# Performance work log

Hardware: AMD Instinct MI355X
Metric: run time of the kernel (lower is better)

Reference implementation:

```python
import jax, jax.numpy as jnp
import numpy as np

HIDDEN = 1024
HEADS = 16
HEAD_DIM = HIDDEN // HEADS
B, S = 2, 2048


def setup_inputs() -> dict:
    key = jax.random.key(0)
    ks = jax.random.split(key, 11)
    std = 1.0 / np.sqrt(HIDDEN)
    return {
        "query": jax.random.normal(ks[0], (B, S, HIDDEN), dtype=jnp.float32),
        "key": jax.random.normal(ks[1], (B, S, HIDDEN), dtype=jnp.float32),
        "value": jax.random.normal(ks[2], (B, S, HIDDEN), dtype=jnp.float32),
        "Wq": jax.random.uniform(ks[3], (HIDDEN, HIDDEN), jnp.float32, -std, std),
        "bq": jax.random.uniform(ks[4], (HIDDEN,), jnp.float32, -std, std),
        "Wk": jax.random.uniform(ks[5], (HIDDEN, HIDDEN), jnp.float32, -std, std),
        "bk": jax.random.uniform(ks[6], (HIDDEN,), jnp.float32, -std, std),
        "Wv": jax.random.uniform(ks[7], (HIDDEN, HIDDEN), jnp.float32, -std, std),
        "bv": jax.random.uniform(ks[8], (HIDDEN,), jnp.float32, -std, std),
        "Wo": jax.random.uniform(ks[9], (HIDDEN, HIDDEN), jnp.float32, -std, std),
        "bo": jax.random.uniform(ks[10], (HIDDEN,), jnp.float32, -std, std),
    }


def reference(query, key, value, Wq, bq, Wk, bk, Wv, bv, Wo, bo):
    b = query.shape[0]
    scale = jnp.sqrt(jnp.float32(HEAD_DIM))
    # linear projections (torch Linear: x @ W.T + b), split into heads -> [b, h, s, d]
    def proj(x, W, bias):
        y = x @ W.T + bias
        return y.reshape(b, -1, HEADS, HEAD_DIM).transpose(0, 2, 1, 3)
    Q = proj(query, Wq, bq)
    K = proj(key, Wk, bk)
    V = proj(value, Wv, bv)
    scores = jnp.einsum("bhqd,bhkd->bhqk", Q, K) / scale
    attn = jax.nn.softmax(scores, axis=-1)
    ctx = jnp.einsum("bhqk,bhkd->bhqd", attn, V)
    ctx = ctx.transpose(0, 2, 1, 3).reshape(b, -1, HIDDEN)
    return ctx @ Wo.T + bo
```

## Files before the change

### kernel.cpp

```cpp
#include <hip/hip_runtime.h>

typedef __attribute__((ext_vector_type(8))) short short8;
typedef __attribute__((ext_vector_type(4))) float float4_t;
typedef __attribute__((ext_vector_type(4))) unsigned int uint4_t;
typedef __attribute__((ext_vector_type(2))) unsigned int uint2_t;
typedef unsigned short u16;

#define HIDDEN 1024
#define HDIM   64
#define SS     2048
#define TOK    4096
#define QSCALE 0.1803368801111137f

__device__ __forceinline__ unsigned int fbits(float f) {
  unsigned int x; __builtin_memcpy(&x, &f, 4); return x;
}
__device__ __forceinline__ u16 f2bf(float f) {
  return (u16)((fbits(f) + 0x8000u) >> 16);
}
__device__ __forceinline__ unsigned int pk2bf(float a, float b) {
  return __builtin_amdgcn_perm(fbits(b) + 0x8000u, fbits(a) + 0x8000u, 0x07060302);
}
__device__ __forceinline__ unsigned int pk2bf_t(float a, float b) {
  return __builtin_amdgcn_perm(fbits(b), fbits(a), 0x07060302);
}

__device__ __forceinline__ void gl_lds16(const u16* g, u16* l) {
  __builtin_amdgcn_global_load_lds(
      (const __attribute__((address_space(1))) unsigned int*)g,
      (__attribute__((address_space(3))) unsigned int*)l, 16, 0, 0);
}

__global__ __launch_bounds__(256) void convert_w(
    const float* __restrict__ w0, const float* __restrict__ w1,
    const float* __restrict__ w2, const float* __restrict__ w3,
    u16* __restrict__ out) {
  int g = (blockIdx.x * 256 + threadIdx.x) * 8;
  int which = g >> 20;
  int off = g & 0xFFFFF;
  const float* src = which == 0 ? w0 : which == 1 ? w1 : which == 2 ? w2 : w3;
  float4_t a = *(const float4_t*)(src + off);
  float4_t b = *(const float4_t*)(src + off + 4);
  uint4_t o;
  o.x = pk2bf(a[0], a[1]); o.y = pk2bf(a[2], a[3]);
  o.z = pk2bf(b[0], b[1]); o.w = pk2bf(b[2], b[3]);
  *(uint4_t*)(out + g) = o;
}

__global__ __launch_bounds__(256) void convert_x(
    const float* __restrict__ x0, const float* __restrict__ x1,
    const float* __restrict__ x2, u16* __restrict__ out) {
  int y = blockIdx.y;
  const float* src = y == 0 ? x0 : y == 1 ? x1 : x2;
  u16* dst = out + ((size_t)y << 22);
  int g = (blockIdx.x * 256 + threadIdx.x) * 8;
  float4_t a = *(const float4_t*)(src + g);
  float4_t b = *(const float4_t*)(src + g + 4);
  uint4_t o;
  o.x = pk2bf(a[0], a[1]); o.y = pk2bf(a[2], a[3]);
  o.z = pk2bf(b[0], b[1]); o.w = pk2bf(b[2], b[3]);
  *(uint4_t*)(dst + g) = o;
}

template<int MTILES, bool AXF32, bool OUTF32>
__device__ __forceinline__ void gemm_bt_body(
    const void* __restrict__ X, const u16* __restrict__ Wb,
    const float* __restrict__ bias, void* __restrict__ Y, int mode, float oscale,
    u16* sA, u16* sB, int row0, int col0) {
  const int tid  = threadIdx.x;
  const int wv   = tid >> 6, lane = tid & 63, quad = lane >> 4, ln = lane & 15;
  const int wm   = (wv >> 1) * (MTILES * 16), wn = (wv & 1) * 64;
  constexpr int AITERS = MTILES / 2;

  float4_t acc[MTILES][4];
#pragma unroll
  for (int i = 0; i < MTILES; i++)
#pragma unroll
    for (int j = 0; j < 4; j++) acc[i][j] = (float4_t)0.0f;

  for (int kt = 0; kt < 32; ++kt) {
    const int k0 = kt * 32;
    short8 ax[AITERS];
    if (AXF32) {
#pragma unroll
      for (int i = 0; i < AITERS; i++) {
        int idx = i * 256 + tid, r = idx >> 2, c = idx & 3;
        const float* p = (const float*)X + (size_t)(row0 + r) * HIDDEN + k0 + c * 8;
        float4_t a = *(const float4_t*)p;
        float4_t b = *(const float4_t*)(p + 4);
        union { unsigned int u[4]; short8 s; } x;
        x.u[0] = pk2bf(a[0], a[1]); x.u[1] = pk2bf(a[2], a[3]);
        x.u[2] = pk2bf(b[0], b[1]); x.u[3] = pk2bf(b[2], b[3]);
        ax[i] = x.s;
      }
    }
    __syncthreads();
#pragma unroll
    for (int i = 0; i < 2; i++) {
      int idx = i * 256 + tid, r = idx >> 2, c = idx & 3;
      int gc = c ^ ((r >> 1) & 3);
      gl_lds16(Wb + (size_t)(col0 + r) * HIDDEN + k0 + gc * 8, sB + idx * 8);
    }
    if (AXF32) {
#pragma unroll
      for (int i = 0; i < AITERS; i++) {
        int idx = i * 256 + tid, r = idx >> 2, c = idx & 3;
        int pos = c ^ ((r >> 1) & 3);
        *(short8*)(sA + r * 32 + pos * 8) = ax[i];
      }
    } else {
#pragma unroll
      for (int i = 0; i < AITERS; i++) {
        int idx = i * 256 + tid, r = idx >> 2, c = idx & 3;
        int gc = c ^ ((r >> 1) & 3);
        gl_lds16((const u16*)X + (size_t)(row0 + r) * HIDDEN + k0 + gc * 8, sA + idx * 8);
      }
    }
    __syncthreads();

    short8 af[MTILES], bfr[4];
#pragma unroll
    for (int mt = 0; mt < MTILES; mt++) {
      int r = wm + mt * 16 + ln;
      int pos = quad ^ ((r >> 1) & 3);
      af[mt] = *(const short8*)(sA + r * 32 + pos * 8);
    }
#pragma unroll
    for (int nt = 0; nt < 4; nt++) {
      int r = wn + nt * 16 + ln;
      int pos = quad ^ ((r >> 1) & 3);
      bfr[nt] = *(const short8*)(sB + r * 32 + pos * 8);
    }
#pragma unroll
    for (int mt = 0; mt < MTILES; mt++)
#pragma unroll
      for (int nt = 0; nt < 4; nt++)
        acc[mt][nt] = __builtin_amdgcn_mfma_f32_16x16x32_bf16(af[mt], bfr[nt], acc[mt][nt], 0, 0, 0);
  }

  float bcol[4];
#pragma unroll
  for (int nt = 0; nt < 4; nt++) bcol[nt] = bias[col0 + wn + nt * 16 + ln];
#pragma unroll
  for (int mt = 0; mt < MTILES; mt++)
#pragma unroll
    for (int nt = 0; nt < 4; nt++) {
      int n = col0 + wn + nt * 16 + ln;
#pragma unroll
      for (int r = 0; r < 4; r++) {
        int m = row0 + wm + mt * 16 + quad * 4 + r;
        float v = (acc[mt][nt][r] + bcol[nt]) * oscale;
        if (mode == 0) {
          if (OUTF32) ((float*)Y)[(size_t)m * HIDDEN + n] = v;
          else        ((u16*)Y)[(size_t)m * HIDDEN + n] = f2bf(v);
        } else {
          ((u16*)Y)[((size_t)(m >> 11) * HIDDEN + n) * SS + (m & 2047)] = f2bf(v);
        }
      }
    }
}

__global__ __launch_bounds__(256) void qkv_gemm_bf16(
    const u16* __restrict__ Xall, const u16* __restrict__ Wall,
    const float* __restrict__ bq, const float* __restrict__ bk, const float* __restrict__ bv,
    u16* __restrict__ Qp, u16* __restrict__ Kp, u16* __restrict__ Vt) {
  __shared__ u16 sA[128 * 32];
  __shared__ u16 sB[128 * 32];
  int z = blockIdx.z;
  const u16* X = Xall + ((size_t)z << 22);
  const u16* W = Wall + ((size_t)z << 20);
  const float* Bp = z == 0 ? bq : z == 1 ? bk : bv;
  u16* Y = z == 0 ? Qp : z == 1 ? Kp : Vt;
  int mode = (z == 2) ? 1 : 0;
  float sc = (z == 0) ? QSCALE : 1.0f;
  gemm_bt_body<4, false, false>(X, W, Bp, Y, mode, sc, sA, sB, blockIdx.y * 128, blockIdx.x * 128);
}

__global__ __launch_bounds__(256) void qkv_gemm_f32(
    const float* __restrict__ xq, const float* __restrict__ xk, const float* __restrict__ xv,
    const u16* __restrict__ Wall,
    const float* __restrict__ bq, const float* __restrict__ bk, const float* __restrict__ bv,
    u16* __restrict__ Qp, u16* __restrict__ Kp, u16* __restrict__ Vt) {
  __shared__ u16 sA[128 * 32];
  __shared__ u16 sB[128 * 32];
  int z = blockIdx.z;
  const float* X = z == 0 ? xq : z == 1 ? xk : xv;
  const u16* W = Wall + ((size_t)z << 20);
  const float* Bp = z == 0 ? bq : z == 1 ? bk : bv;
  u16* Y = z == 0 ? Qp : z == 1 ? Kp : Vt;
  int mode = (z == 2) ? 1 : 0;
  float sc = (z == 0) ? QSCALE : 1.0f;
  gemm_bt_body<4, true, false>(X, W, Bp, Y, mode, sc, sA, sB, blockIdx.y * 128, blockIdx.x * 128);
}

__global__ __launch_bounds__(256) void out_gemm(
    const u16* __restrict__ X, const u16* __restrict__ Wob,
    const float* __restrict__ bias, float* __restrict__ Y) {
  __shared__ u16 sA[64 * 32];
  __shared__ u16 sB[128 * 32];
  gemm_bt_body<2, false, true>(X, Wob, bias, Y, 0, 1.0f, sA, sB, blockIdx.y * 64, blockIdx.x * 128);
}

__global__ __launch_bounds__(256) void attn(
    const u16* __restrict__ Qp, const u16* __restrict__ Kp,
    const u16* __restrict__ Vt, u16* __restrict__ Ctx) {
  __shared__ u16 sK[128 * 64];
  __shared__ u16 sV[80 * 128];
  __shared__ u16 sP[4 * 32 * 64];
  const int tid  = threadIdx.x;
  const int wv   = tid >> 6, lane = tid & 63, quad = lane >> 4, ln = lane & 15;
  const int qt = blockIdx.x, h = blockIdx.y, b = blockIdx.z;
  const int row0 = qt * 128 + wv * 32;

  {
    int rr = 64 + (tid >> 4), cc = (tid & 15) * 8;
    short8 vv;
#pragma unroll
    for (int j = 0; j < 8; j++) vv[j] = (rr == 64) ? (short)0x3F80 : (short)0;
    *(short8*)(sV + rr * 128 + cc) = vv;
  }

  short8 qf[2][2];
#pragma unroll
  for (int j = 0; j < 2; j++)
#pragma unroll
    for (int kk = 0; kk < 2; kk++)
      qf[j][kk] = *(const short8*)(Qp + (size_t)(b * SS + row0 + j * 16 + ln) * HIDDEN
                                   + h * HDIM + kk * 32 + quad * 8);

  float4_t oacc[2][5];
#pragma unroll
  for (int j = 0; j < 2; j++)
#pragma unroll
    for (int t = 0; t < 5; t++) oacc[j][t] = (float4_t)0.f;

  u16* myP = sP + wv * 32 * 64;

  for (int kt = 0; kt < 16; ++kt) {
    __syncthreads();
#pragma unroll
    for (int p = 0; p < 4; p++) {
      int off = p * 256 + tid;
      { int r = off >> 3, c = off & 7;  int gc = c ^ (r & 7);
        gl_lds16(Kp + (size_t)(b * SS + kt * 128 + r) * HIDDEN + h * HDIM + gc * 8, sK + off * 8); }
      { int r = off >> 4, c = off & 15; int gc = c ^ (r & 15);
        gl_lds16(Vt + ((size_t)b * HIDDEN + h * HDIM + r) * SS + kt * 128 + gc * 8, sV + off * 8); }
    }
    __syncthreads();

#pragma unroll
    for (int half = 0; half < 2; half++) {
      float4_t st[4][2];
#pragma unroll
      for (int nt4 = 0; nt4 < 4; nt4++) {
        int nt = half * 4 + nt4;
#pragma unroll
        for (int j = 0; j < 2; j++) st[nt4][j] = (float4_t)0.f;
#pragma unroll
        for (int kk = 0; kk < 2; kk++) {
          int r = nt * 16 + ln;
          int ch = kk * 4 + quad;
          short8 kfr = *(const short8*)(sK + r * 64 + (ch ^ (r & 7)) * 8);
#pragma unroll
          for (int j = 0; j < 2; j++)
            st[nt4][j] = __builtin_amdgcn_mfma_f32_16x16x32_bf16(kfr, qf[j][kk], st[nt4][j], 0, 0, 0);
        }
      }

#pragma unroll
      for (int nt4 = 0; nt4 < 4; nt4++)
#pragma unroll
        for (int j = 0; j < 2; j++) {
          float p0 = __builtin_amdgcn_exp2f(fminf(st[nt4][j][0], 80.f));
          float p1 = __builtin_amdgcn_exp2f(fminf(st[nt4][j][1], 80.f));
          float p2 = __builtin_amdgcn_exp2f(fminf(st[nt4][j][2], 80.f));
          float p3 = __builtin_amdgcn_exp2f(fminf(st[nt4][j][3], 80.f));
          uint2_t w; w.x = pk2bf_t(p0, p1); w.y = pk2bf_t(p2, p3);
          int row = j * 16 + ln;
          int c2 = nt4 * 2 + (quad >> 1);
          int pos = c2 ^ (row & 7);
          *(uint2_t*)(myP + row * 64 + pos * 8 + (quad & 1) * 4) = w;
        }

#pragma unroll
      for (int ks = 0; ks < 2; ks++) {
        int CH = half * 8 + ks * 4 + quad;
        short8 vf[5];
#pragma unroll
        for (int dt = 0; dt < 5; dt++) {
          int d = dt * 16 + ln;
          vf[dt] = *(const short8*)(sV + d * 128 + ((CH ^ (d & 15))) * 8);
        }
#pragma unroll
        for (int j = 0; j < 2; j++) {
          int row = j * 16 + ln;
          int c2 = ks * 4 + quad;
          short8 pb = *(const short8*)(myP + row * 64 + (c2 ^ (row & 7)) * 8);
#pragma unroll
          for (int dt = 0; dt < 5; dt++)
            oacc[j][dt] = __builtin_amdgcn_mfma_f32_16x16x32_bf16(vf[dt], pb, oacc[j][dt], 0, 0, 0);
        }
      }
    }
  }

#pragma unroll
  for (int j = 0; j < 2; j++) {
    float inv = 1.0f / __shfl(oacc[j][4][0], ln, 64);
#pragma unroll
    for (int dt = 0; dt < 4; dt++) {
      uint2_t w;
      w.x = pk2bf(oacc[j][dt][0] * inv, oacc[j][dt][1] * inv);
      w.y = pk2bf(oacc[j][dt][2] * inv, oacc[j][dt][3] * inv);
      int row = j * 16 + ln;
      int ch = dt * 2 + (quad >> 1);
      int pos = ch ^ (row & 7);
      *(uint2_t*)(myP + row * 64 + pos * 8 + (quad & 1) * 4) = w;
    }
  }
#pragma unroll
  for (int jr = 0; jr < 2; jr++)
#pragma unroll
    for (int jc = 0; jc < 2; jc++) {
      int q = lane >> 2;
      int row = jr * 16 + q;
      int c = jc * 4 + (lane & 3);
      int pos = c ^ (row & 7);
      short8 o8 = *(const short8*)(myP + row * 64 + pos * 8);
      *(short8*)(Ctx + (size_t)(b * SS + row0 + row) * HIDDEN + h * HDIM + c * 8) = o8;
    }
}

extern "C" void kernel_launch(void* const* d_in, const int* in_sizes, int n_in,
                              void* d_out, int out_size, void* d_ws, size_t ws_size,
                              hipStream_t stream) {
  const float* q  = (const float*)d_in[0];
  const float* k  = (const float*)d_in[1];
  const float* v  = (const float*)d_in[2];
  const float* Wq = (const float*)d_in[3];
  const float* bq = (const float*)d_in[4];
  const float* Wk = (const float*)d_in[5];
  const float* bk = (const float*)d_in[6];
  const float* Wv = (const float*)d_in[7];
  const float* bv = (const float*)d_in[8];
  const float* Wo = (const float*)d_in[9];
  const float* bo = (const float*)d_in[10];

  u16* Qp   = (u16*)d_ws;
  u16* Kp   = Qp + (size_t)TOK * HIDDEN;
  u16* Vt   = Kp + (size_t)TOK * HIDDEN;
  u16* Wall = Vt + (size_t)TOK * HIDDEN;
  u16* Xall = Wall + (4u << 20);
  u16* Cx   = Qp;
  bool useX = ws_size >= (size_t)56 * 1024 * 1024;

  dim3 blk(256);
  hipLaunchKernelGGL(convert_w, dim3(2048), blk, 0, stream, Wq, Wk, Wv, Wo, Wall);
  if (useX) {
    hipLaunchKernelGGL(convert_x, dim3(2048, 3), blk, 0, stream, q, k, v, Xall);
    hipLaunchKernelGGL(qkv_gemm_bf16, dim3(8, 32, 3), blk, 0, stream,
                       Xall, Wall, bq, bk, bv, Qp, Kp, Vt);
  } else {
    hipLaunchKernelGGL(qkv_gemm_f32, dim3(8, 32, 3), blk, 0, stream,
                       q, k, v, Wall, bq, bk, bv, Qp, Kp, Vt);
  }
  hipLaunchKernelGGL(attn, dim3(16, 16, 2), blk, 0, stream, Qp, Kp, Vt, Cx);
  hipLaunchKernelGGL(out_gemm, dim3(8, 64, 1), blk, 0, stream,
                     Cx, Wall + (3u << 20), bo, (float*)d_out);
}
```

Baseline: 235.8 us.

## Double GEMM K-tile to 64 and merge weight/input conversion kernels

Raises the GEMM K-step per iteration from 32 to 64. This halves the number of loop iterations and barrier pairs and issues two MFMA k-slices per LDS load phase, with the XOR swizzle widened to 8 chunks. It also merges the weight and activation fp32-to-bf16 conversion kernels into a single launch to save one kernel launch. In exchange, each block uses twice as much shared memory, which may reduce occupancy, and the fused conversion grid launches idle blocks for the weight rows.

Result: no change. 234.7 us (-0.5%).

```diff
diff --git a/kernel.cpp b/kernel.cpp
--- a/kernel.cpp
+++ b/kernel.cpp
@@ -31,28 +31,21 @@
       (__attribute__((address_space(3))) unsigned int*)l, 16, 0, 0);
 }
 
-__global__ __launch_bounds__(256) void convert_w(
+__global__ __launch_bounds__(256) void convert_all(
     const float* __restrict__ w0, const float* __restrict__ w1,
     const float* __restrict__ w2, const float* __restrict__ w3,
-    u16* __restrict__ out) {
-  int g = (blockIdx.x * 256 + threadIdx.x) * 8;
-  int which = g >> 20;
-  int off = g & 0xFFFFF;
-  const float* src = which == 0 ? w0 : which == 1 ? w1 : which == 2 ? w2 : w3;
-  float4_t a = *(const float4_t*)(src + off);
-  float4_t b = *(const float4_t*)(src + off + 4);
-  uint4_t o;
-  o.x = pk2bf(a[0], a[1]); o.y = pk2bf(a[2], a[3]);
-  o.z = pk2bf(b[0], b[1]); o.w = pk2bf(b[2], b[3]);
-  *(uint4_t*)(out + g) = o;
-}
-
-__global__ __launch_bounds__(256) void convert_x(
     const float* __restrict__ x0, const float* __restrict__ x1,
-    const float* __restrict__ x2, u16* __restrict__ out) {
+    const float* __restrict__ x2, u16* __restrict__ Wall, u16* __restrict__ Xall) {
   int y = blockIdx.y;
-  const float* src = y == 0 ? x0 : y == 1 ? x1 : x2;
-  u16* dst = out + ((size_t)y << 22);
+  const float* src; u16* dst;
+  if (y < 4) {
+    if (blockIdx.x >= 512) return;
+    src = y == 0 ? w0 : y == 1 ? w1 : y == 2 ? w2 : w3;
+    dst = Wall + ((size_t)y << 20);
+  } else {
+    src = y == 4 ? x0 : y == 5 ? x1 : x2;
+    dst = Xall + ((size_t)(y - 4) << 22);
+  }
   int g = (blockIdx.x * 256 + threadIdx.x) * 8;
   float4_t a = *(const float4_t*)(src + g);
   float4_t b = *(const float4_t*)(src + g + 4);
@@ -70,7 +63,7 @@
   const int tid  = threadIdx.x;
   const int wv   = tid >> 6, lane = tid & 63, quad = lane >> 4, ln = lane & 15;
   const int wm   = (wv >> 1) * (MTILES * 16), wn = (wv & 1) * 64;
-  constexpr int AITERS = MTILES / 2;
+  constexpr int AITERS = MTILES;
 
   float4_t acc[MTILES][4];
 #pragma unroll
@@ -78,13 +71,13 @@
 #pragma unroll
     for (int j = 0; j < 4; j++) acc[i][j] = (float4_t)0.0f;
 
-  for (int kt = 0; kt < 32; ++kt) {
-    const int k0 = kt * 32;
+  for (int kt = 0; kt < 16; ++kt) {
+    const int k0 = kt * 64;
     short8 ax[AITERS];
     if (AXF32) {
 #pragma unroll
       for (int i = 0; i < AITERS; i++) {
-        int idx = i * 256 + tid, r = idx >> 2, c = idx & 3;
+        int idx = i * 256 + tid, r = idx >> 3, c = idx & 7;
         const float* p = (const float*)X + (size_t)(row0 + r) * HIDDEN + k0 + c * 8;
         float4_t a = *(const float4_t*)p;
         float4_t b = *(const float4_t*)(p + 4);
@@ -96,46 +89,52 @@
     }
     __syncthreads();
 #pragma unroll
-    for (int i = 0; i < 2; i++) {
-      int idx = i * 256 + tid, r = idx >> 2, c = idx & 3;
-      int gc = c ^ ((r >> 1) & 3);
+    for (int i = 0; i < 4; i++) {
+      int idx = i * 256 + tid, r = idx >> 3, c = idx & 7;
+      int gc = c ^ (r & 7);
       gl_lds16(Wb + (size_t)(col0 + r) * HIDDEN + k0 + gc * 8, sB + idx * 8);
     }
     if (AXF32) {
 #pragma unroll
       for (int i = 0; i < AITERS; i++) {
-        int idx = i * 256 + tid, r = idx >> 2, c = idx & 3;
-        int pos = c ^ ((r >> 1) & 3);
-        *(short8*)(sA + r * 32 + pos * 8) = ax[i];
+        int idx = i * 256 + tid, r = idx >> 3, c = idx & 7;
+        int pos = c ^ (r & 7);
+        *(short8*)(sA + r * 64 + pos * 8) = ax[i];
       }
     } else {
 #pragma unroll
       for (int i = 0; i < AITERS; i++) {
-        int idx = i * 256 + tid, r = idx >> 2, c = idx & 3;
-        int gc = c ^ ((r >> 1) & 3);
+        int idx = i * 256 + tid, r = idx >> 3, c = idx & 7;
+        int gc = c ^ (r & 7);
         gl_lds16((const u16*)X + (size_t)(row0 + r) * HIDDEN + k0 + gc * 8, sA + idx * 8);
       }
     }
     __syncthreads();
 
-    short8 af[MTILES], bfr[4];
-#pragma unroll
-    for (int mt = 0; mt < MTILES; mt++) {
-      int r = wm + mt * 16 + ln;
-      int pos = quad ^ ((r >> 1) & 3);
-      af[mt] = *(const short8*)(sA + r * 32 + pos * 8);
-    }
-#pragma unroll
-    for (int nt = 0; nt < 4; nt++) {
-      int r = wn + nt * 16 + ln;
-      int pos = quad ^ ((r >> 1) & 3);
-      bfr[nt] = *(const short8*)(sB + r * 32 + pos * 8);
-    }
+    short8 af[MTILES][2], bfr[4][2];
 #pragma unroll
     for (int mt = 0; mt < MTILES; mt++)
 #pragma unroll
-      for (int nt = 0; nt < 4; nt++)
-        acc[mt][nt] = __builtin_amdgcn_mfma_f32_16x16x32_bf16(af[mt], bfr[nt], acc[mt][nt], 0, 0, 0);
+      for (int kk = 0; kk < 2; kk++) {
+        int r = wm + mt * 16 + ln;
+        int ch = kk * 4 + quad;
+        af[mt][kk] = *(const short8*)(sA + r * 64 + (ch ^ (r & 7)) * 8);
+      }
+#pragma unroll
+    for (int nt = 0; nt < 4; nt++)
+#pragma unroll
+      for (int kk = 0; kk < 2; kk++) {
+        int r = wn + nt * 16 + ln;
+        int ch = kk * 4 + quad;
+        bfr[nt][kk] = *(const short8*)(sB + r * 64 + (ch ^ (r & 7)) * 8);
+      }
+#pragma unroll
+    for (int kk = 0; kk < 2; kk++)
+#pragma unroll
+      for (int mt = 0; mt < MTILES; mt++)
+#pragma unroll
+        for (int nt = 0; nt < 4; nt++)
+          acc[mt][nt] = __builtin_amdgcn_mfma_f32_16x16x32_bf16(af[mt][kk], bfr[nt][kk], acc[mt][nt], 0, 0, 0);
   }
 
   float bcol[4];
@@ -164,8 +163,8 @@
     const u16* __restrict__ Xall, const u16* __restrict__ Wall,
     const float* __restrict__ bq, const float* __restrict__ bk, const float* __restrict__ bv,
     u16* __restrict__ Qp, u16* __restrict__ Kp, u16* __restrict__ Vt) {
-  __shared__ u16 sA[128 * 32];
-  __shared__ u16 sB[128 * 32];
+  __shared__ u16 sA[128 * 64];
+  __shared__ u16 sB[128 * 64];
   int z = blockIdx.z;
   const u16* X = Xall + ((size_t)z << 22);
   const u16* W = Wall + ((size_t)z << 20);
@@ -181,8 +180,8 @@
     const u16* __restrict__ Wall,
     const float* __restrict__ bq, const float* __restrict__ bk, const float* __restrict__ bv,
     u16* __restrict__ Qp, u16* __restrict__ Kp, u16* __restrict__ Vt) {
-  __shared__ u16 sA[128 * 32];
-  __shared__ u16 sB[128 * 32];
+  __shared__ u16 sA[128 * 64];
+  __shared__ u16 sB[128 * 64];
   int z = blockIdx.z;
   const float* X = z == 0 ? xq : z == 1 ? xk : xv;
   const u16* W = Wall + ((size_t)z << 20);
@@ -196,8 +195,8 @@
 __global__ __launch_bounds__(256) void out_gemm(
     const u16* __restrict__ X, const u16* __restrict__ Wob,
     const float* __restrict__ bias, float* __restrict__ Y) {
-  __shared__ u16 sA[64 * 32];
-  __shared__ u16 sB[128 * 32];
+  __shared__ u16 sA[64 * 64];
+  __shared__ u16 sB[128 * 64];
   gemm_bt_body<2, false, true>(X, Wob, bias, Y, 0, 1.0f, sA, sB, blockIdx.y * 64, blockIdx.x * 128);
 }
 
@@ -355,12 +354,14 @@
   bool useX = ws_size >= (size_t)56 * 1024 * 1024;
 
   dim3 blk(256);
-  hipLaunchKernelGGL(convert_w, dim3(2048), blk, 0, stream, Wq, Wk, Wv, Wo, Wall);
   if (useX) {
-    hipLaunchKernelGGL(convert_x, dim3(2048, 3), blk, 0, stream, q, k, v, Xall);
+    hipLaunchKernelGGL(convert_all, dim3(2048, 7), blk, 0, stream,
+                       Wq, Wk, Wv, Wo, q, k, v, Wall, Xall);
     hipLaunchKernelGGL(qkv_gemm_bf16, dim3(8, 32, 3), blk, 0, stream,
                        Xall, Wall, bq, bk, bv, Qp, Kp, Vt);
   } else {
+    hipLaunchKernelGGL(convert_all, dim3(512, 4), blk, 0, stream,
+                       Wq, Wk, Wv, Wo, q, k, v, Wall, Wall);
     hipLaunchKernelGGL(qkv_gemm_f32, dim3(8, 32, 3), blk, 0, stream,
                        q, k, v, Wall, bq, bk, bv, Qp, Kp, Vt);
   }
```
